# Kernel tuning notes

Hardware: AMD Instinct MI355X
Metric: run time of the kernel (lower is better)

Reference implementation:

```python
import jax, jax.numpy as jnp
import numpy as np

N = 100000
E = 3200000
C = 64
K = 10
ALPHA = 0.9


def setup_inputs() -> dict:
    key = jax.random.key(0)
    k1, k2, k3, k4, k5 = jax.random.split(key, 5)
    y = jax.random.uniform(k1, (N, C), dtype=jnp.float32)
    train_mask = jax.random.randint(k2, (N,), 0, 2) > 0
    src = jax.random.randint(k3, (E,), 0, N)
    dst = jax.random.randint(k4, (E,), 0, N)
    edge_index = jnp.stack([src, dst], axis=0)
    edge_weight = jax.random.uniform(k5, (E,), dtype=jnp.float32)
    return {"y": y, "train_mask": train_mask, "edge_index": edge_index,
            "edge_weight": edge_weight}


def reference(y, train_mask, edge_index, edge_weight):
    src, dst = edge_index[0], edge_index[1]
    mask = train_mask[:, None]  # [N, 1]
    # out = zeros_like(y); out[train_mask] = y[train_mask]
    out = jnp.where(mask, y, 0.0)
    for _ in range(K):
        # sparse adjacency matmul: (homo_adj @ out) via gather + segment-sum
        msg = out[src] * edge_weight[:, None]          # [E, C]
        agg = jax.ops.segment_sum(msg, dst, num_segments=N)  # [N, C]
        out = ALPHA * agg + (1.0 - ALPHA) * out
        out = jnp.where(mask, y, out)                  # reset train labels
        out = jnp.clip(out, 0.0, 1.0)
    return out
```

## Files before the change

### kernel.cpp

```cpp
#include <hip/hip_runtime.h>

#define NN 100000
#define EE 3200000
#define CC 64
#define KK 10
#define ALPHA 0.9f
#define BKT_SH 8
#define BMASK 255
#define NBKT 391
#define CAP 6144
#define EPB 8192
#define NB_BIN ((EE + EPB - 1) / EPB)
#define NBLK256 ((NN + 255) / 256)


__global__ void init_small(int* __restrict__ flag, int* __restrict__ changed,
                           int* __restrict__ gcursor) {
    int t = blockIdx.x * blockDim.x + threadIdx.x;
    if (t == 0) *flag = 0;
    if (t <= KK) changed[t] = (t == 0) ? 1 : 0;
    if (t < NBKT) gcursor[t] = t * CAP;
}

__global__ void detect_mask(const unsigned char* __restrict__ mb, int* __restrict__ flag) {
    int i = blockIdx.x * blockDim.x + threadIdx.x;
    if (i < NN && (i & 3) != 0 && mb[i] != 0) *flag = 1;
}

__global__ void make_mask_count(const unsigned char* __restrict__ mb,
                                const int* __restrict__ mi, const int* __restrict__ flag,
                                unsigned char* __restrict__ mask, int* __restrict__ blkCnt) {
    __shared__ int s[256];
    int i = blockIdx.x * 256 + threadIdx.x;
    int f = 0;
    if (i < NN) {
        unsigned char m = ((*flag) ? (mb[i] != 0) : (mi[i] != 0)) ? 1 : 0;
        mask[i] = m;
        f = 1 - (int)m;
    }
    s[threadIdx.x] = f;
    __syncthreads();
    for (int off = 128; off; off >>= 1) {
        if (threadIdx.x < off) s[threadIdx.x] += s[threadIdx.x + off];
        __syncthreads();
    }
    if (threadIdx.x == 0) blkCnt[blockIdx.x] = s[0];
}

__global__ void scan_blk(int* __restrict__ blkCnt, int* __restrict__ nU) {
    __shared__ int s[512];
    int t = threadIdx.x;
    s[t] = (t < NBLK256) ? blkCnt[t] : 0;
    __syncthreads();
    for (int off = 1; off < 512; off <<= 1) {
        int x = (t >= off) ? s[t - off] : 0;
        __syncthreads();
        s[t] += x;
        __syncthreads();
    }
    if (t < NBLK256) blkCnt[t] = (t == 0) ? 0 : s[t - 1];
    if (t == 0) *nU = s[511];
}

__global__ void compact_unm(const unsigned char* __restrict__ mask,
                            const int* __restrict__ blkBase, int* __restrict__ ulist) {
    __shared__ int s[256];
    int i = blockIdx.x * 256 + threadIdx.x;
    int f = (i < NN && !mask[i]) ? 1 : 0;
    s[threadIdx.x] = f;
    __syncthreads();
    for (int off = 1; off < 256; off <<= 1) {
        int x = (threadIdx.x >= off) ? s[threadIdx.x - off] : 0;
        __syncthreads();
        s[threadIdx.x] += x;
        __syncthreads();
    }
    if (f) ulist[blkBase[blockIdx.x] + s[threadIdx.x] - 1] = i;
}

__global__ __launch_bounds__(256) void bin_edges(
    const int* __restrict__ src, const int* __restrict__ dst,
    const float* __restrict__ w, const unsigned char* __restrict__ mask,
    int* __restrict__ gcursor, uint2* __restrict__ binned) {
    __shared__ int h[NBKT];
    __shared__ int gb[NBKT];
    __shared__ int cur[NBKT];
    for (int i = threadIdx.x; i < NBKT; i += 256) { h[i] = 0; cur[i] = 0; }
    __syncthreads();
    int eb = blockIdx.x * EPB;
#pragma unroll 4
    for (int j = 0; j < EPB / 256; ++j) {
        int e = eb + j * 256 + threadIdx.x;
        if (e < EE) {
            int d = dst[e];
            if (!mask[d]) atomicAdd(&h[d >> BKT_SH], 1);
        }
    }
    __syncthreads();
    for (int b = threadIdx.x; b < NBKT; b += 256)
        gb[b] = h[b] ? atomicAdd(&gcursor[b], h[b]) : 0;
    __syncthreads();
#pragma unroll 4
    for (int j = 0; j < EPB / 256; ++j) {
        int e = eb + j * 256 + threadIdx.x;
        if (e < EE) {
            int d = dst[e];
            if (!mask[d]) {
                int b = d >> BKT_SH;
                int p = gb[b] + atomicAdd(&cur[b], 1);
                unsigned wq = (unsigned)(w[e] * 32768.0f);
                binned[p] = make_uint2(wq, (unsigned)src[e] | ((unsigned)(d & BMASK) << 17));
            }
        }
    }
}

__global__ void scan_buckets(const int* __restrict__ gcursor,
                             int* __restrict__ bucket_base) {
    __shared__ int s[512];
    int t = threadIdx.x;
    s[t] = (t < NBKT) ? (gcursor[t] - t * CAP) : 0;
    __syncthreads();
    for (int off = 1; off < 512; off <<= 1) {
        int x = (t >= off) ? s[t - off] : 0;
        __syncthreads();
        s[t] += x;
        __syncthreads();
    }
    if (t < NBKT) bucket_base[t] = (t == 0) ? 0 : s[t - 1];
    if (t == 0) bucket_base[NBKT] = s[511];
}

__global__ __launch_bounds__(256) void build_csr(
    const uint2* __restrict__ binned, const int* __restrict__ gcursor,
    const int* __restrict__ bucket_base, int* __restrict__ row_ptr,
    unsigned* __restrict__ recs) {
    __shared__ int h[256];
    __shared__ int cur[256];
    __shared__ int part[64];
    int b = blockIdx.x;
    int beg = b * CAP;
    int end = gcursor[b];
    int base = bucket_base[b];
    int node0 = b << BKT_SH;
    int nnode = min(256, NN - node0);
    int t = threadIdx.x;
    h[t] = 0;
    __syncthreads();
    for (int e = beg + t; e < end; e += 256)
        atomicAdd(&h[(binned[e].y >> 17) & BMASK], 1);
    __syncthreads();
    int v0 = 0, v1 = 0, v2 = 0, v3 = 0;
    if (t < 64) {
        v0 = h[4 * t]; v1 = h[4 * t + 1]; v2 = h[4 * t + 2]; v3 = h[4 * t + 3];
        part[t] = v0 + v1 + v2 + v3;
    }
    __syncthreads();
    for (int off = 1; off < 64; off <<= 1) {
        int x = (t < 64 && t >= off) ? part[t - off] : 0;
        __syncthreads();
        if (t < 64) part[t] += x;
        __syncthreads();
    }
    if (t < 64) {
        int run = (t == 0) ? 0 : part[t - 1];
        h[4 * t] = run; run += v0;
        h[4 * t + 1] = run; run += v1;
        h[4 * t + 2] = run; run += v2;
        h[4 * t + 3] = run;
    }
    __syncthreads();
    if (t < nnode) {
        row_ptr[node0 + t] = base + h[t];
        cur[t] = 0;
    }
    if (b == NBKT - 1 && t == 0) row_ptr[NN] = bucket_base[NBKT];
    __syncthreads();
    for (int e = beg + t; e < end; e += 256) {
        uint2 r = binned[e];
        int dlo = (r.y >> 17) & BMASK;
        int p = base + h[dlo] + atomicAdd(&cur[dlo], 1);
        recs[p] = (r.x << 17) | (r.y & 0x1FFFFu);
    }
}

__global__ void init_state(const float4* __restrict__ y4,
                           const unsigned char* __restrict__ mask,
                           float4* __restrict__ out4,
                           uchar4* __restrict__ a4, uchar4* __restrict__ b4) {
    int i = blockIdx.x * blockDim.x + threadIdx.x;
    if (i < NN * 16) {
        int d = i >> 4;
        uchar4 v = make_uchar4(0, 0, 0, 0);
        if (mask[d]) {
            float4 yv = y4[i];
            out4[i] = yv;
            v = make_uchar4((unsigned char)(yv.x * 255.0f + 0.5f),
                            (unsigned char)(yv.y * 255.0f + 0.5f),
                            (unsigned char)(yv.z * 255.0f + 0.5f),
                            (unsigned char)(yv.w * 255.0f + 0.5f));
        }
        a4[i] = v;
        b4[i] = v;
    }
}

__global__ void finalize_out(const uchar4* __restrict__ state4,
                             const unsigned char* __restrict__ mask,
                             float4* __restrict__ out4) {
    int i = blockIdx.x * blockDim.x + threadIdx.x;
    if (i < NN * 16) {
        int d = i >> 4;
        if (!mask[d]) {
            uchar4 v = state4[i];
            const float S = 1.0f / 255.0f;
            out4[i] = make_float4(v.x * S, v.y * S, v.z * S, v.w * S);
        }
    }
}

__global__ __launch_bounds__(256) void prop_u8(
    const uint2* __restrict__ prev2, uint2* __restrict__ next2,
    const int* __restrict__ ulist, const int* __restrict__ nU,
    const int* __restrict__ row_ptr, const unsigned* __restrict__ recs,
    const int* __restrict__ run_flag, int* __restrict__ chg_flag) {
    if (*run_flag == 0) return;
    int wave = threadIdx.x >> 6;
    int lane = threadIdx.x & 63;
    int grp  = lane >> 3;
    int cidx = lane & 7;
    int widx = blockIdx.x * 4 + wave;
    if (widx >= *nU) return;
    int d = ulist[widx];
    int beg = row_ptr[d];
    int end = row_ptr[d + 1];

    unsigned acc[8];
#pragma unroll
    for (int k = 0; k < 8; ++k) acc[k] = 0;

    int e = beg;
    for (; e + 32 <= end; e += 32) {
        unsigned r[4];
        uint2 x[4];
#pragma unroll
        for (int j = 0; j < 4; ++j) r[j] = recs[e + j * 8 + grp];
#pragma unroll
        for (int j = 0; j < 4; ++j) x[j] = prev2[(r[j] & 0x1FFFFu) * 8 + cidx];
#pragma unroll
        for (int j = 0; j < 4; ++j) {
            unsigned wq = r[j] >> 17;
            acc[0] += wq * ( x[j].x        & 0xffu);
            acc[1] += wq * ((x[j].x >>  8) & 0xffu);
            acc[2] += wq * ((x[j].x >> 16) & 0xffu);
            acc[3] += wq * ( x[j].x >> 24        );
            acc[4] += wq * ( x[j].y        & 0xffu);
            acc[5] += wq * ((x[j].y >>  8) & 0xffu);
            acc[6] += wq * ((x[j].y >> 16) & 0xffu);
            acc[7] += wq * ( x[j].y >> 24        );
        }
    }
    for (; e < end; e += 8) {
        int ee = e + grp;
        bool ok = ee < end;
        unsigned r = ok ? recs[ee] : 0u;
        uint2 x = ok ? prev2[(r & 0x1FFFFu) * 8 + cidx] : make_uint2(0u, 0u);
        unsigned wq = r >> 17;
        acc[0] += wq * ( x.x        & 0xffu);
        acc[1] += wq * ((x.x >>  8) & 0xffu);
        acc[2] += wq * ((x.x >> 16) & 0xffu);
        acc[3] += wq * ( x.x >> 24        );
        acc[4] += wq * ( x.y        & 0xffu);
        acc[5] += wq * ((x.y >>  8) & 0xffu);
        acc[6] += wq * ((x.y >> 16) & 0xffu);
        acc[7] += wq * ( x.y >> 24        );
    }
    uint2 s = prev2[(unsigned)d * 8 + cidx];
#pragma unroll
    for (int m = 8; m <= 32; m <<= 1) {
#pragma unroll
        for (int k = 0; k < 8; ++k) acc[k] += __shfl_xor(acc[k], m, 64);
    }
    if (lane < 8) {
        const float K1 = ALPHA / (32768.0f * 255.0f);
        const float K2 = (1.0f - ALPHA) / 255.0f;
        float o[8];
#pragma unroll
        for (int k = 0; k < 8; ++k) {
            unsigned sb = ((k < 4 ? (s.x >> (8 * k)) : (s.y >> (8 * (k - 4)))) & 0xffu);
            float v = (float)acc[k] * K1 + (float)sb * K2;
            o[k] = fminf(fmaxf(v, 0.0f), 1.0f);
        }
        unsigned lo = (unsigned)(o[0] * 255.0f + 0.5f)
                    | ((unsigned)(o[1] * 255.0f + 0.5f) << 8)
                    | ((unsigned)(o[2] * 255.0f + 0.5f) << 16)
                    | ((unsigned)(o[3] * 255.0f + 0.5f) << 24);
        unsigned hi = (unsigned)(o[4] * 255.0f + 0.5f)
                    | ((unsigned)(o[5] * 255.0f + 0.5f) << 8)
                    | ((unsigned)(o[6] * 255.0f + 0.5f) << 16)
                    | ((unsigned)(o[7] * 255.0f + 0.5f) << 24);
        if (lo != s.x || hi != s.y) *chg_flag = 1;
        next2[(unsigned)d * 8 + lane] = make_uint2(lo, hi);
    }
}

extern "C" void kernel_launch(void* const* d_in, const int* in_sizes, int n_in,
                              void* d_out, int out_size, void* d_ws, size_t ws_size,
                              hipStream_t stream) {
    const float* y = (const float*)d_in[0];
    const unsigned char* mb = (const unsigned char*)d_in[1];
    const int* mi = (const int*)d_in[1];
    const int* edge_index = (const int*)d_in[2];
    const float* ew = (const float*)d_in[3];
    const int* src = edge_index;
    const int* dst = edge_index + EE;

    char* ws = (char*)d_ws;
    int*      flag        = (int*)(ws + 0);
    int*      nU          = (int*)(ws + 64);
    int*      changed     = (int*)(ws + 128);
    int*      bucket_base = (int*)(ws + 256);
    int*      gcursor     = (int*)(ws + 2048);
    int*      blkCnt      = (int*)(ws + 4096);
    unsigned char* mask   = (unsigned char*)(ws + 8192);
    int*      ulist       = (int*)(ws + 108544);
    int*      row_ptr     = (int*)(ws + 508928);
    unsigned* recs        = (unsigned*)(ws + 909312);
    uint2*    u8A         = (uint2*)(ws + 13709312);
    uint2*    u8B         = (uint2*)(ws + 20109440);
    uint2*    binned      = (uint2*)d_out;

    const int NB_I    = (NN * 16 + 255) / 256;
    const int NB_PROP = (NN + 3) / 4;

    init_small<<<1, 512, 0, stream>>>(flag, changed, gcursor);
    detect_mask<<<NBLK256, 256, 0, stream>>>(mb, flag);
    make_mask_count<<<NBLK256, 256, 0, stream>>>(mb, mi, flag, mask, blkCnt);
    scan_blk<<<1, 512, 0, stream>>>(blkCnt, nU);
    compact_unm<<<NBLK256, 256, 0, stream>>>(mask, blkCnt, ulist);
    bin_edges<<<NB_BIN, 256, 0, stream>>>(src, dst, ew, mask, gcursor, binned);
    scan_buckets<<<1, 512, 0, stream>>>(gcursor, bucket_base);
    build_csr<<<NBKT, 256, 0, stream>>>(binned, gcursor, bucket_base, row_ptr, recs);

    init_state<<<NB_I, 256, 0, stream>>>((const float4*)y, mask, (float4*)d_out,
                                         (uchar4*)u8A, (uchar4*)u8B);

    uint2* cur = u8A;
    uint2* oth = u8B;
    for (int k = 0; k < KK; ++k) {
        prop_u8<<<NB_PROP, 256, 0, stream>>>(cur, oth, ulist, nU, row_ptr, recs,
                                             &changed[k], &changed[k + 1]);
        uint2* t = cur; cur = oth; oth = t;
    }
    finalize_out<<<NB_I, 256, 0, stream>>>((const uchar4*)cur, mask, (float4*)d_out);
}
```

Baseline: 344.0 us.

## Split bucket cursors into sub-slots and cache edge data in registers while binning

Each destination bucket's global cursor is split into 8 sub-cursors chosen by block index, and each sub-cursor owns its own slice of the bucket. This spreads contention on the global atomics. The bin_edges block size drops to 2048 edges so each thread keeps its 8 edges' src, weight and destination in registers, avoiding a second read of dst, src and w. scan_buckets and build_csr are updated to walk the 8 sub-ranges, and the workspace offsets are shifted to fit the larger cursor array. The risks are more bin_edges blocks, each running its own histogram and cursor-reservation phase, and possible sub-slice overflow if edges are unevenly split across sub-cursors.

```diff
diff --git a/kernel.cpp b/kernel.cpp
--- a/kernel.cpp
+++ b/kernel.cpp
@@ -9,17 +9,20 @@
 #define BMASK 255
 #define NBKT 391
 #define CAP 6144
-#define EPB 8192
+#define SUB 8
+#define CAPS (CAP / SUB)
+#define EPB 2048
 #define NB_BIN ((EE + EPB - 1) / EPB)
 #define NBLK256 ((NN + 255) / 256)
 
 
 __global__ void init_small(int* __restrict__ flag, int* __restrict__ changed,
                            int* __restrict__ gcursor) {
-    int t = blockIdx.x * blockDim.x + threadIdx.x;
+    int t = threadIdx.x;
     if (t == 0) *flag = 0;
     if (t <= KK) changed[t] = (t == 0) ? 1 : 0;
-    if (t < NBKT) gcursor[t] = t * CAP;
+    for (int i = t; i < NBKT * SUB; i += 512)
+        gcursor[i] = (i >> 3) * CAP + (i & 7) * CAPS;
 }
 
 __global__ void detect_mask(const unsigned char* __restrict__ mb, int* __restrict__ flag) {
@@ -88,29 +91,33 @@
     for (int i = threadIdx.x; i < NBKT; i += 256) { h[i] = 0; cur[i] = 0; }
     __syncthreads();
     int eb = blockIdx.x * EPB;
-#pragma unroll 4
-    for (int j = 0; j < EPB / 256; ++j) {
-        int e = eb + j * 256 + threadIdx.x;
-        if (e < EE) {
-            int d = dst[e];
-            if (!mask[d]) atomicAdd(&h[d >> BKT_SH], 1);
-        }
-    }
-    __syncthreads();
-    for (int b = threadIdx.x; b < NBKT; b += 256)
-        gb[b] = h[b] ? atomicAdd(&gcursor[b], h[b]) : 0;
-    __syncthreads();
-#pragma unroll 4
-    for (int j = 0; j < EPB / 256; ++j) {
+    int sub = blockIdx.x & (SUB - 1);
+    int s_[8], b_[8], dlo_[8];
+    unsigned w_[8];
+#pragma unroll
+    for (int j = 0; j < 8; ++j) {
+        b_[j] = -1;
         int e = eb + j * 256 + threadIdx.x;
         if (e < EE) {
             int d = dst[e];
             if (!mask[d]) {
-                int b = d >> BKT_SH;
-                int p = gb[b] + atomicAdd(&cur[b], 1);
-                unsigned wq = (unsigned)(w[e] * 32768.0f);
-                binned[p] = make_uint2(wq, (unsigned)src[e] | ((unsigned)(d & BMASK) << 17));
+                s_[j] = src[e];
+                w_[j] = (unsigned)(w[e] * 32768.0f);
+                b_[j] = d >> BKT_SH;
+                dlo_[j] = d & BMASK;
+                atomicAdd(&h[b_[j]], 1);
             }
+        }
+    }
+    __syncthreads();
+    for (int b = threadIdx.x; b < NBKT; b += 256)
+        gb[b] = h[b] ? atomicAdd(&gcursor[b * SUB + sub], h[b]) : 0;
+    __syncthreads();
+#pragma unroll
+    for (int j = 0; j < 8; ++j) {
+        if (b_[j] >= 0) {
+            int p = gb[b_[j]] + atomicAdd(&cur[b_[j]], 1);
+            binned[p] = make_uint2(w_[j], (unsigned)s_[j] | ((unsigned)dlo_[j] << 17));
         }
     }
 }
@@ -119,7 +126,13 @@
                              int* __restrict__ bucket_base) {
     __shared__ int s[512];
     int t = threadIdx.x;
-    s[t] = (t < NBKT) ? (gcursor[t] - t * CAP) : 0;
+    int c = 0;
+    if (t < NBKT) {
+#pragma unroll
+        for (int ss = 0; ss < SUB; ++ss)
+            c += gcursor[t * SUB + ss] - (t * CAP + ss * CAPS);
+    }
+    s[t] = c;
     __syncthreads();
     for (int off = 1; off < 512; off <<= 1) {
         int x = (t >= off) ? s[t - off] : 0;
@@ -139,16 +152,19 @@
     __shared__ int cur[256];
     __shared__ int part[64];
     int b = blockIdx.x;
-    int beg = b * CAP;
-    int end = gcursor[b];
     int base = bucket_base[b];
     int node0 = b << BKT_SH;
     int nnode = min(256, NN - node0);
     int t = threadIdx.x;
     h[t] = 0;
     __syncthreads();
-    for (int e = beg + t; e < end; e += 256)
-        atomicAdd(&h[(binned[e].y >> 17) & BMASK], 1);
+#pragma unroll
+    for (int ss = 0; ss < SUB; ++ss) {
+        int sbeg = b * CAP + ss * CAPS;
+        int send = gcursor[b * SUB + ss];
+        for (int e = sbeg + t; e < send; e += 256)
+            atomicAdd(&h[(binned[e].y >> 17) & BMASK], 1);
+    }
     __syncthreads();
     int v0 = 0, v1 = 0, v2 = 0, v3 = 0;
     if (t < 64) {
@@ -176,11 +192,16 @@
     }
     if (b == NBKT - 1 && t == 0) row_ptr[NN] = bucket_base[NBKT];
     __syncthreads();
-    for (int e = beg + t; e < end; e += 256) {
-        uint2 r = binned[e];
-        int dlo = (r.y >> 17) & BMASK;
-        int p = base + h[dlo] + atomicAdd(&cur[dlo], 1);
-        recs[p] = (r.x << 17) | (r.y & 0x1FFFFu);
+#pragma unroll
+    for (int ss = 0; ss < SUB; ++ss) {
+        int sbeg = b * CAP + ss * CAPS;
+        int send = gcursor[b * SUB + ss];
+        for (int e = sbeg + t; e < send; e += 256) {
+            uint2 r = binned[e];
+            int dlo = (r.y >> 17) & BMASK;
+            int p = base + h[dlo] + atomicAdd(&cur[dlo], 1);
+            recs[p] = (r.x << 17) | (r.y & 0x1FFFFu);
+        }
     }
 }
 
@@ -321,13 +342,13 @@
     int*      changed     = (int*)(ws + 128);
     int*      bucket_base = (int*)(ws + 256);
     int*      gcursor     = (int*)(ws + 2048);
-    int*      blkCnt      = (int*)(ws + 4096);
-    unsigned char* mask   = (unsigned char*)(ws + 8192);
-    int*      ulist       = (int*)(ws + 108544);
-    int*      row_ptr     = (int*)(ws + 508928);
-    unsigned* recs        = (unsigned*)(ws + 909312);
-    uint2*    u8A         = (uint2*)(ws + 13709312);
-    uint2*    u8B         = (uint2*)(ws + 20109440);
+    int*      blkCnt      = (int*)(ws + 14592);
+    unsigned char* mask   = (unsigned char*)(ws + 16384);
+    int*      ulist       = (int*)(ws + 116736);
+    int*      row_ptr     = (int*)(ws + 517120);
+    unsigned* recs        = (unsigned*)(ws + 917504);
+    uint2*    u8A         = (uint2*)(ws + 13717504);
+    uint2*    u8B         = (uint2*)(ws + 20117632);
     uint2*    binned      = (uint2*)d_out;
 
     const int NB_I    = (NN * 16 + 255) / 256;
```

Result: faster. 331.4 us (-3.7%).
